# Performance work log

Hardware: AMD Instinct MI355X
Metric: run time of the kernel (lower is better)

## Reference

```python
import jax, jax.numpy as jnp
import numpy as np

NUM_EXPERT = 8
IN_FEAT = 512
OUT_FEAT = 512
TOKENS = 16384


def setup_inputs() -> dict:
    key = jax.random.key(0)
    k_inp, k_gate, k_w = jax.random.split(key, 3)
    inp = jax.random.uniform(k_inp, (TOKENS, IN_FEAT), dtype=jnp.float32)
    gate = jax.random.randint(k_gate, (TOKENS,), 0, NUM_EXPERT, dtype=jnp.int32)
    # nn.Linear-style init: U(-1/sqrt(in_feat), 1/sqrt(in_feat))
    bound = 1.0 / np.sqrt(IN_FEAT)
    weight = jax.random.uniform(
        k_w, (NUM_EXPERT, OUT_FEAT, IN_FEAT), dtype=jnp.float32,
        minval=-bound, maxval=bound)
    return {"inp": inp, "gate": gate, "weight": weight}


def reference(inp, gate, weight):
    # y_t = weight[gate[t]] @ x_t  (per-token expert-specific GEMM)
    # Implemented via one-hot dispatch to avoid gathering a [T, O, I] weight tensor.
    num_expert = weight.shape[0]
    dispatch = jax.nn.one_hot(gate, num_expert, dtype=inp.dtype)  # [T, E]
    xe = jnp.einsum('te,ti->eti', dispatch, inp)                  # [E, T, I]
    ye = jnp.einsum('eti,eoi->eto', xe, weight)                   # [E, T, O]
    out = jnp.einsum('eto,te->to', ye, dispatch)                  # [T, O]
    return out
```

## Files before the change

kernel.cpp:

```cpp
#include <hip/hip_runtime.h>
#include <hip/hip_bf16.h>

#define TOKENS 16384
#define NEXP 8
#define INF 512
#define OUTF 512

#define BM 64
#define BN 128
#define BK 32
#define NST (INF / BK)
#define MAXMT 40
#define EROWS (MAXMT * BM)

using f32x4 = __attribute__((ext_vector_type(4))) float;
using bfrag = __attribute__((ext_vector_type(8))) __bf16;
using s8v   = __attribute__((ext_vector_type(8))) short;

__device__ __forceinline__ short f2bf(float f) {
  union { float f; unsigned u; } v; v.f = f;
  unsigned r = v.u + 0x7fffu + ((v.u >> 16) & 1u);
  return (short)(r >> 16);
}

__device__ __forceinline__ void gload16(const void* g, void* l) {
  __builtin_amdgcn_global_load_lds(
      (const __attribute__((address_space(1))) unsigned int*)g,
      (__attribute__((address_space(3))) unsigned int*)l, 16, 0, 0);
}

__device__ __forceinline__ s8v pack8(float4 a, float4 b) {
  s8v p;
  p[0] = f2bf(a.x); p[1] = f2bf(a.y); p[2] = f2bf(a.z); p[3] = f2bf(a.w);
  p[4] = f2bf(b.x); p[5] = f2bf(b.y); p[6] = f2bf(b.z); p[7] = f2bf(b.w);
  return p;
}

__device__ __forceinline__ bfrag cvt8(f32x4 lo, f32x4 hi) {
  bfrag r;
  r[0] = (__bf16)lo[0]; r[1] = (__bf16)lo[1];
  r[2] = (__bf16)lo[2]; r[3] = (__bf16)lo[3];
  r[4] = (__bf16)hi[0]; r[5] = (__bf16)hi[1];
  r[6] = (__bf16)hi[2]; r[7] = (__bf16)hi[3];
  return r;
}

__global__ void k_prep(const int* __restrict__ gate, int* __restrict__ cursor,
                       int* __restrict__ perm, const float* __restrict__ w,
                       s8v* __restrict__ wb) {
  __shared__ int lc[NEXP], lb[NEXP];
  const int bid = blockIdx.x, tid = threadIdx.x;
  if (bid < 64) {
    if (tid < NEXP) lc[tid] = 0;
    __syncthreads();
    int t = bid * 256 + tid;
    int e = gate[t];
    int ls = atomicAdd(&lc[e], 1);
    __syncthreads();
    if (tid < NEXP) lb[tid] = lc[tid] ? atomicAdd(&cursor[tid], lc[tid]) : 0;
    __syncthreads();
    perm[e * EROWS + lb[e] + ls] = t;
  } else {
    int idx = (bid - 64) * 256 + tid;
    const float4* src = (const float4*)w + (size_t)idx * 2;
    wb[idx] = pack8(src[0], src[1]);
  }
}

#define KBAR(N)                                                         \
  asm volatile("s_waitcnt vmcnt(" #N ") lgkmcnt(0)" ::: "memory");      \
  __builtin_amdgcn_sched_barrier(0);                                    \
  __builtin_amdgcn_s_barrier();                                         \
  __builtin_amdgcn_sched_barrier(0);

__global__ __launch_bounds__(256, 3)
void moe_gemm8(const float* __restrict__ inp, const short* __restrict__ wbf,
               const int* __restrict__ cursor, const int* __restrict__ perm,
               float* __restrict__ out) {
  const int bid = blockIdx.x;
  const int e  = bid & 7;
  const int nt = (bid >> 3) & 3;
  const int mt = bid >> 5;
  const int cnt = cursor[e];
  if (mt * BM >= cnt) return;
  const int m_valid = min(BM, cnt - mt * BM);
  const int* pb = perm + e * EROWS + mt * BM;

  __shared__ __align__(16) char Albs[3][BM * BK * 4];
  __shared__ __align__(16) char Blbs[3][BN * BK * 2];
  __shared__ int toks[BM];

  const int tid = threadIdx.x;
  if (tid < BM) toks[tid] = pb[(tid < m_valid) ? tid : 0];
  __syncthreads();

  const int lane = tid & 63;
  const int wid  = tid >> 6;
  const int wr = wid >> 1, wc = wid & 1;
  const int lr = lane & 15;
  const int lg = lane >> 4;

  const float* agp[2];
#pragma unroll
  for (int s = 0; s < 2; s++) {
    int row  = s * 32 + (tid >> 3);
    int clog = (tid & 7) ^ (row & 7);
    agp[s] = inp + (size_t)toks[row] * INF + clog * 4;
  }

  const short* Wbase = wbf + ((size_t)e * OUTF + (size_t)nt * BN) * INF;
  const short* bgp[2];
#pragma unroll
  for (int s = 0; s < 2; s++) {
    int row  = s * 64 + (tid >> 2);
    int clog = (tid & 3) ^ (row & 3);
    bgp[s] = Wbase + (size_t)row * INF + clog * 8;
  }

  f32x4 acc[2][4];
#pragma unroll
  for (int m = 0; m < 2; m++)
#pragma unroll
    for (int j = 0; j < 4; j++) acc[m][j] = (f32x4)0.0f;

#define DMA(t_)                                                               \
  {                                                                           \
    char* ab_ = (char*)Albs[(t_) % 3];                                        \
    char* bb_ = (char*)Blbs[(t_) % 3];                                        \
    gload16(agp[0] + (t_) * BK, ab_ + tid * 16);                              \
    gload16(agp[1] + (t_) * BK, ab_ + 4096 + tid * 16);                       \
    gload16(bgp[0] + (t_) * BK, bb_ + tid * 16);                              \
    gload16(bgp[1] + (t_) * BK, bb_ + 4096 + tid * 16);                       \
  }
#define COMP(t_)                                                              \
  {                                                                           \
    const char* ab_ = (const char*)Albs[(t_) % 3];                            \
    const char* bb_ = (const char*)Blbs[(t_) % 3];                            \
    bfrag af[2], bv[4];                                                       \
    _Pragma("unroll") for (int m = 0; m < 2; m++) {                           \
      int row = wr * 32 + m * 16 + lr;                                        \
      int c0 = (lg * 2) ^ (row & 7), c1 = (lg * 2 + 1) ^ (row & 7);           \
      f32x4 lo = *(const f32x4*)(ab_ + row * 128 + c0 * 16);                  \
      f32x4 hi = *(const f32x4*)(ab_ + row * 128 + c1 * 16);                  \
      af[m] = cvt8(lo, hi);                                                   \
    }                                                                         \
    _Pragma("unroll") for (int j = 0; j < 4; j++) {                           \
      int row = wc * 64 + j * 16 + lr;                                        \
      int c = lg ^ (row & 3);                                                 \
      bv[j] = *(const bfrag*)(bb_ + row * 64 + c * 16);                       \
    }                                                                         \
    _Pragma("unroll") for (int m = 0; m < 2; m++)                             \
      _Pragma("unroll") for (int j = 0; j < 4; j++)                           \
          acc[m][j] = __builtin_amdgcn_mfma_f32_16x16x32_bf16(                \
              af[m], bv[j], acc[m][j], 0, 0, 0);                              \
  }

  DMA(0);
  DMA(1);
  KBAR(4)

#pragma unroll
  for (int t = 0; t < NST; t++) {
    if (t + 2 < NST) DMA(t + 2);
    COMP(t);
    if (t + 2 < NST) {
      KBAR(4)
    } else if (t + 1 < NST) {
      KBAR(0)
    }
  }

#pragma unroll
  for (int m = 0; m < 2; m++) {
#pragma unroll
    for (int r = 0; r < 4; r++) {
      int rowE = wr * 32 + m * 16 + lg * 4 + r;
      if (rowE < m_valid) {
        float* orow = out + (size_t)toks[rowE] * OUTF + (size_t)nt * BN +
                      (size_t)wc * 64 + lr;
#pragma unroll
        for (int j = 0; j < 4; j++) orow[j * 16] = acc[m][j][r];
      }
    }
  }
#undef DMA
#undef COMP
}

extern "C" void kernel_launch(void* const* d_in, const int* in_sizes, int n_in,
                              void* d_out, int out_size, void* d_ws, size_t ws_size,
                              hipStream_t stream) {
  (void)in_sizes; (void)n_in; (void)out_size; (void)ws_size;
  const float* inp    = (const float*)d_in[0];
  const int*   gate   = (const int*)d_in[1];
  const float* weight = (const float*)d_in[2];
  float* out = (float*)d_out;

  char* ws = (char*)d_ws;
  int*   cursor = (int*)ws;
  int*   perm   = (int*)(ws + 4096);
  short* wbf    = (short*)(ws + (1 << 20));

  hipMemsetAsync(cursor, 0, 64, stream);
  k_prep<<<64 + (NEXP * OUTF * INF) / (256 * 8), 256, 0, stream>>>(
      gate, cursor, perm, weight, (s8v*)wbf);
  moe_gemm8<<<NEXP * 4 * MAXMT, 256, 0, stream>>>(inp, wbf, cursor, perm, out);
}
```

Before: 37.93 us.

## Pre-convert activations to bf16 and double the M tile to 128

The prep kernel now also converts the fp32 input to bf16 in workspace, so the GEMM loads bf16 A tiles directly and no longer converts fp32 to bf16 inside the inner loop. The M tile grows from 64 to 128 rows (4x4 MFMA accumulators per wave, launch bounds lowered to 2 blocks), which reuses each weight tile across more tokens. The cost is an extra full pass that reads the input and writes a bf16 copy, plus fewer blocks in flight and more wasted rows in partially filled expert tiles. With MAXMT 20 and BM 128, per-expert capacity stays at 2560 tokens.

New measurement: 39.38 us. 1.04x slower.

```diff
diff --git a/kernel.cpp b/kernel.cpp
--- a/kernel.cpp
+++ b/kernel.cpp
@@ -6,12 +6,14 @@
 #define INF 512
 #define OUTF 512
 
-#define BM 64
+#define BM 128
 #define BN 128
 #define BK 32
 #define NST (INF / BK)
-#define MAXMT 40
+#define MAXMT 20
 #define EROWS (MAXMT * BM)
+#define SLOTA (BM * BK * 2)
+#define SLOTB (BN * BK * 2)
 
 using f32x4 = __attribute__((ext_vector_type(4))) float;
 using bfrag = __attribute__((ext_vector_type(8))) __bf16;
@@ -36,18 +38,10 @@
   return p;
 }
 
-__device__ __forceinline__ bfrag cvt8(f32x4 lo, f32x4 hi) {
-  bfrag r;
-  r[0] = (__bf16)lo[0]; r[1] = (__bf16)lo[1];
-  r[2] = (__bf16)lo[2]; r[3] = (__bf16)lo[3];
-  r[4] = (__bf16)hi[0]; r[5] = (__bf16)hi[1];
-  r[6] = (__bf16)hi[2]; r[7] = (__bf16)hi[3];
-  return r;
-}
-
 __global__ void k_prep(const int* __restrict__ gate, int* __restrict__ cursor,
                        int* __restrict__ perm, const float* __restrict__ w,
-                       s8v* __restrict__ wb) {
+                       s8v* __restrict__ wb, const float* __restrict__ inp,
+                       s8v* __restrict__ inpb) {
   __shared__ int lc[NEXP], lb[NEXP];
   const int bid = blockIdx.x, tid = threadIdx.x;
   if (bid < 64) {
@@ -60,10 +54,14 @@
     if (tid < NEXP) lb[tid] = lc[tid] ? atomicAdd(&cursor[tid], lc[tid]) : 0;
     __syncthreads();
     perm[e * EROWS + lb[e] + ls] = t;
-  } else {
+  } else if (bid < 1088) {
     int idx = (bid - 64) * 256 + tid;
     const float4* src = (const float4*)w + (size_t)idx * 2;
     wb[idx] = pack8(src[0], src[1]);
+  } else {
+    int idx = (bid - 1088) * 256 + tid;
+    const float4* src = (const float4*)inp + (size_t)idx * 2;
+    inpb[idx] = pack8(src[0], src[1]);
   }
 }
 
@@ -73,10 +71,10 @@
   __builtin_amdgcn_s_barrier();                                         \
   __builtin_amdgcn_sched_barrier(0);
 
-__global__ __launch_bounds__(256, 3)
-void moe_gemm8(const float* __restrict__ inp, const short* __restrict__ wbf,
-               const int* __restrict__ cursor, const int* __restrict__ perm,
-               float* __restrict__ out) {
+__global__ __launch_bounds__(256, 2)
+void moe_gemm11(const short* __restrict__ inpb, const short* __restrict__ wbf,
+                const int* __restrict__ cursor, const int* __restrict__ perm,
+                float* __restrict__ out) {
   const int bid = blockIdx.x;
   const int e  = bid & 7;
   const int nt = (bid >> 3) & 3;
@@ -86,8 +84,8 @@
   const int m_valid = min(BM, cnt - mt * BM);
   const int* pb = perm + e * EROWS + mt * BM;
 
-  __shared__ __align__(16) char Albs[3][BM * BK * 4];
-  __shared__ __align__(16) char Blbs[3][BN * BK * 2];
+  __shared__ __align__(16) char Albs[3][SLOTA];
+  __shared__ __align__(16) char Blbs[3][SLOTB];
   __shared__ int toks[BM];
 
   const int tid = threadIdx.x;
@@ -100,12 +98,12 @@
   const int lr = lane & 15;
   const int lg = lane >> 4;
 
-  const float* agp[2];
+  const short* agp[2];
 #pragma unroll
   for (int s = 0; s < 2; s++) {
-    int row  = s * 32 + (tid >> 3);
-    int clog = (tid & 7) ^ (row & 7);
-    agp[s] = inp + (size_t)toks[row] * INF + clog * 4;
+    int row  = s * 64 + (tid >> 2);
+    int clog = (tid & 3) ^ (row & 3);
+    agp[s] = inpb + (size_t)toks[row] * INF + clog * 8;
   }
 
   const short* Wbase = wbf + ((size_t)e * OUTF + (size_t)nt * BN) * INF;
@@ -117,11 +115,11 @@
     bgp[s] = Wbase + (size_t)row * INF + clog * 8;
   }
 
-  f32x4 acc[2][4];
-#pragma unroll
-  for (int m = 0; m < 2; m++)
-#pragma unroll
-    for (int j = 0; j < 4; j++) acc[m][j] = (f32x4)0.0f;
+  f32x4 acc[4][4];
+#pragma unroll
+  for (int i = 0; i < 4; i++)
+#pragma unroll
+    for (int j = 0; j < 4; j++) acc[i][j] = (f32x4)0.0f;
 
 #define DMA(t_)                                                               \
   {                                                                           \
@@ -136,23 +134,21 @@
   {                                                                           \
     const char* ab_ = (const char*)Albs[(t_) % 3];                            \
     const char* bb_ = (const char*)Blbs[(t_) % 3];                            \
-    bfrag af[2], bv[4];                                                       \
-    _Pragma("unroll") for (int m = 0; m < 2; m++) {                           \
-      int row = wr * 32 + m * 16 + lr;                                        \
-      int c0 = (lg * 2) ^ (row & 7), c1 = (lg * 2 + 1) ^ (row & 7);           \
-      f32x4 lo = *(const f32x4*)(ab_ + row * 128 + c0 * 16);                  \
-      f32x4 hi = *(const f32x4*)(ab_ + row * 128 + c1 * 16);                  \
-      af[m] = cvt8(lo, hi);                                                   \
+    bfrag af[4], bv[4];                                                       \
+    _Pragma("unroll") for (int i = 0; i < 4; i++) {                           \
+      int row = wr * 64 + i * 16 + lr;                                        \
+      int c = lg ^ (row & 3);                                                 \
+      af[i] = *(const bfrag*)(ab_ + row * 64 + c * 16);                       \
     }                                                                         \
     _Pragma("unroll") for (int j = 0; j < 4; j++) {                           \
       int row = wc * 64 + j * 16 + lr;                                        \
       int c = lg ^ (row & 3);                                                 \
       bv[j] = *(const bfrag*)(bb_ + row * 64 + c * 16);                       \
     }                                                                         \
-    _Pragma("unroll") for (int m = 0; m < 2; m++)                             \
+    _Pragma("unroll") for (int i = 0; i < 4; i++)                             \
       _Pragma("unroll") for (int j = 0; j < 4; j++)                           \
-          acc[m][j] = __builtin_amdgcn_mfma_f32_16x16x32_bf16(                \
-              af[m], bv[j], acc[m][j], 0, 0, 0);                              \
+          acc[i][j] = __builtin_amdgcn_mfma_f32_16x16x32_bf16(                \
+              af[i], bv[j], acc[i][j], 0, 0, 0);                              \
   }
 
   DMA(0);
@@ -171,15 +167,16 @@
   }
 
 #pragma unroll
-  for (int m = 0; m < 2; m++) {
+  for (int i = 0; i < 4; i++) {
+    int rbase = wr * 64 + i * 16 + lg * 4;
 #pragma unroll
     for (int r = 0; r < 4; r++) {
-      int rowE = wr * 32 + m * 16 + lg * 4 + r;
-      if (rowE < m_valid) {
-        float* orow = out + (size_t)toks[rowE] * OUTF + (size_t)nt * BN +
+      int rr = rbase + r;
+      if (rr < m_valid) {
+        float* orow = out + (size_t)toks[rr] * OUTF + (size_t)nt * BN +
                       (size_t)wc * 64 + lr;
 #pragma unroll
-        for (int j = 0; j < 4; j++) orow[j * 16] = acc[m][j][r];
+        for (int j = 0; j < 4; j++) orow[j * 16] = acc[i][j][r];
       }
     }
   }
@@ -200,9 +197,10 @@
   int*   cursor = (int*)ws;
   int*   perm   = (int*)(ws + 4096);
   short* wbf    = (short*)(ws + (1 << 20));
+  short* inpb   = (short*)(ws + (8 << 20));
 
   hipMemsetAsync(cursor, 0, 64, stream);
-  k_prep<<<64 + (NEXP * OUTF * INF) / (256 * 8), 256, 0, stream>>>(
-      gate, cursor, perm, weight, (s8v*)wbf);
-  moe_gemm8<<<NEXP * 4 * MAXMT, 256, 0, stream>>>(inp, wbf, cursor, perm, out);
-}
+  k_prep<<<1088 + (TOKENS * INF) / (256 * 8), 256, 0, stream>>>(
+      gate, cursor, perm, weight, (s8v*)wbf, inp, (s8v*)inpb);
+  moe_gemm11<<<NEXP * 4 * MAXMT, 256, 0, stream>>>(inpb, wbf, cursor, perm, out);
+}
```
